# Kernel tuning notes

Hardware: AMD Instinct MI355X
Metric: run time of the kernel (lower is better)

The kernel has to match this reference:

```python
import jax, jax.numpy as jnp
import numpy as np

G = 64      # norm_groups
T = 5       # Newton-Schulz iterations
EPS = 1e-5


def setup_inputs() -> dict:
    key = jax.random.key(0)
    weight = jax.random.normal(key, (2048, 18432), dtype=jnp.float32)
    return {"weight": weight}


def reference(weight):
    out_ch = weight.shape[0]
    # Z: [G, c, d] with c = out_ch // G, d = prod(rest)
    Z = weight.reshape(G, out_ch // G, -1)
    Zc = Z - jnp.mean(Z, axis=-1, keepdims=True)
    # S = Zc @ Zc^T : [G, c, c]
    S = jnp.einsum('gcd,ged->gce', Zc, Zc)
    c = S.shape[-1]
    eye = jnp.eye(c, dtype=S.dtype)
    S = S + EPS * eye
    # Frobenius norm per group, keepdim -> [G,1,1]
    norm_S = jnp.sqrt(jnp.sum(S * S, axis=(1, 2), keepdims=True))
    S = S / norm_S
    # Newton-Schulz: B_{t+1} = 1.5*B_t - 0.5 * B_t^3 @ S
    B = jnp.broadcast_to(eye, S.shape)
    for _ in range(T):
        B3 = jnp.matmul(jnp.matmul(B, B), B)
        B = 1.5 * B - 0.5 * jnp.matmul(B3, S)
    W = jnp.matmul(B, Zc) / jnp.sqrt(norm_S)
    return W.reshape(weight.shape)
```

## Files before the change

kernel.cpp:

```cpp
#include <hip/hip_runtime.h>

#define G 64
#define C 32
#define D 18432
#define NCH 16
#define TD (D / NCH)
#define NST (TD / 128)
#define EPS 1e-5f
#define NS_ITERS 5

typedef __attribute__((ext_vector_type(8))) short short8v;
typedef __attribute__((ext_vector_type(4))) float float4v;

__device__ __forceinline__ void split3(float x, unsigned short& h1,
                                       unsigned short& h2, unsigned short& h3) {
    unsigned int u = __float_as_uint(x);
    unsigned int m1 = u & 0xffff0000u;
    float r1 = x - __uint_as_float(m1);
    unsigned int u2 = __float_as_uint(r1);
    unsigned int m2 = u2 & 0xffff0000u;
    float r2 = r1 - __uint_as_float(m2);
    h1 = (unsigned short)(m1 >> 16);
    h2 = (unsigned short)(m2 >> 16);
    h3 = (unsigned short)(__float_as_uint(r2) >> 16);
}

__device__ __forceinline__ void split8(const float4& v0, const float4& v1,
                                       short8v& p1, short8v& p2, short8v& p3,
                                       float& rs) {
    float x[8] = {v0.x, v0.y, v0.z, v0.w, v1.x, v1.y, v1.z, v1.w};
#pragma unroll
    for (int j = 0; j < 8; ++j) {
        unsigned short h1, h2, h3;
        rs += x[j];
        split3(x[j], h1, h2, h3);
        p1[j] = (short)h1; p2[j] = (short)h2; p3[j] = (short)h3;
    }
}

__global__ __launch_bounds__(256) void k1_gram(const float* __restrict__ W,
                                               float* __restrict__ psum,
                                               float* __restrict__ prow) {
    __shared__ float red[4 * 1056 + 4 * C];

    const int ch   = blockIdx.x;
    const int g    = blockIdx.y;
    const int bid  = g * NCH + ch;
    const int tid  = threadIdx.x;
    const int lane = tid & 63;
    const int wave = tid >> 6;

    const int rbase = lane & 15;
    const int koff  = (lane >> 4) * 8;

    const float* Zg = W + (size_t)g * C * D + (size_t)ch * TD;
    const float* p0 = Zg + (size_t)rbase * D + wave * 32 + koff;
    const float* p1 = p0 + (size_t)16 * D;

    float4v acc[2][2];
#pragma unroll
    for (int a = 0; a < 2; ++a)
#pragma unroll
        for (int b = 0; b < 2; ++b) acc[a][b] = (float4v)0.f;
    float rs0 = 0.f, rs1 = 0.f;

    float4 c00 = *(const float4*)(p0);
    float4 c01 = *(const float4*)(p0 + 4);
    float4 c10 = *(const float4*)(p1);
    float4 c11 = *(const float4*)(p1 + 4);

#pragma unroll
    for (int st = 0; st < NST; ++st) {
        float4 n00, n01, n10, n11;
        if (st + 1 < NST) {
            n00 = *(const float4*)(p0 + (st + 1) * 128);
            n01 = *(const float4*)(p0 + (st + 1) * 128 + 4);
            n10 = *(const float4*)(p1 + (st + 1) * 128);
            n11 = *(const float4*)(p1 + (st + 1) * 128 + 4);
        }
        short8v fa[3], fb[3];
        split8(c00, c01, fa[0], fa[1], fa[2], rs0);
        split8(c10, c11, fb[0], fb[1], fb[2], rs1);

        short8v* fr[2] = {fa, fb};
#pragma unroll
        for (int a = 0; a < 2; ++a)
#pragma unroll
            for (int b = 0; b < 2; ++b) {
                float4v t = acc[a][b];
                t = __builtin_amdgcn_mfma_f32_16x16x32_bf16(fr[a][0], fr[b][0], t, 0, 0, 0);
                t = __builtin_amdgcn_mfma_f32_16x16x32_bf16(fr[a][0], fr[b][1], t, 0, 0, 0);
                t = __builtin_amdgcn_mfma_f32_16x16x32_bf16(fr[a][1], fr[b][0], t, 0, 0, 0);
                t = __builtin_amdgcn_mfma_f32_16x16x32_bf16(fr[a][1], fr[b][1], t, 0, 0, 0);
                t = __builtin_amdgcn_mfma_f32_16x16x32_bf16(fr[a][0], fr[b][2], t, 0, 0, 0);
                t = __builtin_amdgcn_mfma_f32_16x16x32_bf16(fr[a][2], fr[b][0], t, 0, 0, 0);
                acc[a][b] = t;
            }
        c00 = n00; c01 = n01; c10 = n10; c11 = n11;
    }

    rs0 += __shfl_xor(rs0, 16, 64); rs0 += __shfl_xor(rs0, 32, 64);
    rs1 += __shfl_xor(rs1, 16, 64); rs1 += __shfl_xor(rs1, 32, 64);
    if (lane < 16) {
        red[4224 + wave * C + lane]      = rs0;
        red[4224 + wave * C + 16 + lane] = rs1;
    }

#pragma unroll
    for (int a = 0; a < 2; ++a)
#pragma unroll
        for (int b = 0; b < 2; ++b)
#pragma unroll
            for (int j = 0; j < 4; ++j) {
                int row = 16 * a + ((lane >> 4) << 2) + j;
                int col = 16 * b + (lane & 15);
                red[wave * 1056 + row * 33 + col] = acc[a][b][j];
            }
    __syncthreads();

#pragma unroll
    for (int k = 0; k < 4; ++k) {
        int el = tid + 256 * k;
        int row = el >> 5, col = el & 31;
        int o = row * 33 + col;
        float sv = red[o] + red[1056 + o] + red[2112 + o] + red[3168 + o];
        psum[(size_t)bid * (C * C) + el] = sv;
    }
    if (tid < C) {
        float s = red[4224 + tid] + red[4224 + C + tid] +
                  red[4224 + 2 * C + tid] + red[4224 + 3 * C + tid];
        prow[(size_t)bid * C + tid] = s;
    }
}

__global__ __launch_bounds__(256) void k2_ns(const float* __restrict__ psum,
                                             const float* __restrict__ prow,
                                             float* __restrict__ MT,
                                             float* __restrict__ vout) {
    __shared__ float S[C][C + 1];
    __shared__ float B[C][C + 1];
    __shared__ float T1[C][C + 1];
    __shared__ float T2[C][C + 1];
    __shared__ float mean[C];
    __shared__ float redw[4];
    __shared__ float normsh;

    const int g   = blockIdx.x;
    const int tid = threadIdx.x;
    const int e   = tid & 31;
    const int cbq = tid >> 5;

    float selt[4];
#pragma unroll
    for (int k = 0; k < 4; ++k) {
        int el = tid + 256 * k;
        float s = 0.f;
#pragma unroll
        for (int ch = 0; ch < NCH; ++ch)
            s += psum[((size_t)g * NCH + ch) * (C * C) + el];
        selt[k] = s;
    }
    if (tid < C) {
        float s = 0.f;
#pragma unroll
        for (int ch = 0; ch < NCH; ++ch)
            s += prow[((size_t)g * NCH + ch) * C + tid];
        mean[tid] = s / (float)D;
    }
    __syncthreads();

    float ss = 0.f;
#pragma unroll
    for (int k = 0; k < 4; ++k) {
        int el = tid + 256 * k;
        int c = el >> 5;
        float sv = selt[k] - (float)D * mean[c] * mean[e];
        if (c == e) sv += EPS;
        S[c][e] = sv;
        ss = fmaf(sv, sv, ss);
    }
#pragma unroll
    for (int off = 32; off >= 1; off >>= 1) ss += __shfl_xor(ss, off, 64);
    if ((tid & 63) == 0) redw[tid >> 6] = ss;
    __syncthreads();
    if (tid == 0) normsh = sqrtf(redw[0] + redw[1] + redw[2] + redw[3]);
    __syncthreads();
    const float inv_norm = 1.0f / normsh;
#pragma unroll
    for (int k = 0; k < 4; ++k) {
        int c = cbq + 8 * k;
        S[c][e] *= inv_norm;
        B[c][e] = (c == e) ? 1.f : 0.f;
    }
    __syncthreads();

    for (int it = 0; it < NS_ITERS; ++it) {
#pragma unroll
        for (int k = 0; k < 4; ++k) {
            int c = cbq + 8 * k;
            float s = 0.f;
            for (int kk = 0; kk < C; ++kk)
                s = fmaf(B[c][kk], B[kk][e], s);
            T1[c][e] = s;
        }
        __syncthreads();
#pragma unroll
        for (int k = 0; k < 4; ++k) {
            int c = cbq + 8 * k;
            float s = 0.f;
            for (int kk = 0; kk < C; ++kk)
                s = fmaf(T1[c][kk], B[kk][e], s);
            T2[c][e] = s;
        }
        __syncthreads();
        float pv[4];
#pragma unroll
        for (int k = 0; k < 4; ++k) {
            int c = cbq + 8 * k;
            float s = 0.f;
            for (int kk = 0; kk < C; ++kk)
                s = fmaf(T2[c][kk], S[kk][e], s);
            pv[k] = s;
        }
#pragma unroll
        for (int k = 0; k < 4; ++k) {
            int c = cbq + 8 * k;
            B[c][e] = 1.5f * B[c][e] - 0.5f * pv[k];
        }
        __syncthreads();
    }

    const float invs = 1.0f / sqrtf(normsh);
#pragma unroll
    for (int k = 0; k < 4; ++k) {
        int c = cbq + 8 * k;
        MT[(size_t)g * (C * C) + e * C + c] = B[c][e] * invs;
    }
    if (tid < C) {
        float s = 0.f;
        for (int ee = 0; ee < C; ++ee)
            s = fmaf(B[tid][ee] * invs, mean[ee], s);
        vout[(size_t)g * C + tid] = s;
    }
}

__global__ __launch_bounds__(256) void k3_apply(const float* __restrict__ W,
                                                const float* __restrict__ MT,
                                                const float* __restrict__ vv,
                                                float* __restrict__ out) {
    const int blocksPerGroup = D / 512;
    const int g   = blockIdx.x / blocksPerGroup;
    const int cbk = blockIdx.x % blocksPerGroup;
    const int d0  = cbk * 512 + (int)threadIdx.x * 2;
    const float* Zg = W + (size_t)g * C * D + d0;
    const float* Mg = MT + (size_t)g * (C * C);

    float accx[C], accy[C];
#pragma unroll
    for (int r = 0; r < C; ++r) { accx[r] = 0.f; accy[r] = 0.f; }

    for (int e = 0; e < C; ++e) {
        float2 z = *(const float2*)(Zg + (size_t)e * D);
#pragma unroll
        for (int r = 0; r < C; ++r) {
            float m = Mg[e * C + r];
            accx[r] = fmaf(m, z.x, accx[r]);
            accy[r] = fmaf(m, z.y, accy[r]);
        }
    }

    float* Og = out + (size_t)g * C * D + d0;
#pragma unroll
    for (int r = 0; r < C; ++r) {
        float vr = vv[g * C + r];
        float2 o = make_float2(accx[r] - vr, accy[r] - vr);
        double dv;
        __builtin_memcpy(&dv, &o, 8);
        __builtin_nontemporal_store(dv, (double*)(Og + (size_t)r * D));
    }
}

extern "C" void kernel_launch(void* const* d_in, const int* in_sizes, int n_in,
                              void* d_out, int out_size, void* d_ws, size_t ws_size,
                              hipStream_t stream) {
    const float* w = (const float*)d_in[0];
    float* out = (float*)d_out;

    float* psum = (float*)d_ws;
    float* prow = psum + (size_t)(G * NCH) * (C * C);
    float* MT   = prow + (size_t)(G * NCH) * C;
    float* vv   = MT   + (size_t)G * (C * C);

    k1_gram <<<dim3(NCH, G), 256, 0, stream>>>(w, psum, prow);
    k2_ns   <<<G,            256, 0, stream>>>(psum, prow, MT, vv);
    k3_apply<<<G * (D / 512), 256, 0, stream>>>(w, MT, vv, out);
}
```

Baseline: 92.04 us.

## Fuse Newton-Schulz stage into gram kernel via last-block atomic counter

Removes the separate Newton-Schulz kernel. The last block to finish each group's partial Gram sums, detected with a per-group atomic counter after a threadfence, reduces the partials and runs the iteration, reusing the reduction shared memory. A tiny zeroing kernel resets the counters each call. This saves one launch and lets the Newton-Schulz work for early groups overlap Gram computation for other groups. The cost is a serialized tail on the last block per group and reliance on fence ordering for correctness.

```diff
diff --git a/kernel.cpp b/kernel.cpp
--- a/kernel.cpp
+++ b/kernel.cpp
@@ -38,10 +38,19 @@
     }
 }
 
+__global__ void k0_zero(int* __restrict__ cnt) { cnt[threadIdx.x] = 0; }
+
 __global__ __launch_bounds__(256) void k1_gram(const float* __restrict__ W,
                                                float* __restrict__ psum,
-                                               float* __restrict__ prow) {
+                                               float* __restrict__ prow,
+                                               float* __restrict__ MT,
+                                               float* __restrict__ vout,
+                                               int* __restrict__ cnt) {
     __shared__ float red[4 * 1056 + 4 * C];
+    __shared__ float mean[C];
+    __shared__ float redw[4];
+    __shared__ float normsh;
+    __shared__ int lastFlag;
 
     const int ch   = blockIdx.x;
     const int g    = blockIdx.y;
@@ -131,116 +140,117 @@
                   red[4224 + 2 * C + tid] + red[4224 + 3 * C + tid];
         prow[(size_t)bid * C + tid] = s;
     }
-}
-
-__global__ __launch_bounds__(256) void k2_ns(const float* __restrict__ psum,
-                                             const float* __restrict__ prow,
-                                             float* __restrict__ MT,
-                                             float* __restrict__ vout) {
-    __shared__ float S[C][C + 1];
-    __shared__ float B[C][C + 1];
-    __shared__ float T1[C][C + 1];
-    __shared__ float T2[C][C + 1];
-    __shared__ float mean[C];
-    __shared__ float redw[4];
-    __shared__ float normsh;
-
-    const int g   = blockIdx.x;
-    const int tid = threadIdx.x;
-    const int e   = tid & 31;
-    const int cbq = tid >> 5;
-
-    float selt[4];
-#pragma unroll
-    for (int k = 0; k < 4; ++k) {
-        int el = tid + 256 * k;
-        float s = 0.f;
-#pragma unroll
-        for (int ch = 0; ch < NCH; ++ch)
-            s += psum[((size_t)g * NCH + ch) * (C * C) + el];
-        selt[k] = s;
-    }
-    if (tid < C) {
-        float s = 0.f;
-#pragma unroll
-        for (int ch = 0; ch < NCH; ++ch)
-            s += prow[((size_t)g * NCH + ch) * C + tid];
-        mean[tid] = s / (float)D;
-    }
+
     __syncthreads();
-
-    float ss = 0.f;
-#pragma unroll
-    for (int k = 0; k < 4; ++k) {
-        int el = tid + 256 * k;
-        int c = el >> 5;
-        float sv = selt[k] - (float)D * mean[c] * mean[e];
-        if (c == e) sv += EPS;
-        S[c][e] = sv;
-        ss = fmaf(sv, sv, ss);
-    }
-#pragma unroll
-    for (int off = 32; off >= 1; off >>= 1) ss += __shfl_xor(ss, off, 64);
-    if ((tid & 63) == 0) redw[tid >> 6] = ss;
+    if (tid == 0) {
+        __threadfence();
+        int old = atomicAdd(&cnt[g], 1);
+        lastFlag = (old == NCH - 1);
+    }
     __syncthreads();
-    if (tid == 0) normsh = sqrtf(redw[0] + redw[1] + redw[2] + redw[3]);
-    __syncthreads();
-    const float inv_norm = 1.0f / normsh;
-#pragma unroll
-    for (int k = 0; k < 4; ++k) {
-        int c = cbq + 8 * k;
-        S[c][e] *= inv_norm;
-        B[c][e] = (c == e) ? 1.f : 0.f;
-    }
-    __syncthreads();
-
-    for (int it = 0; it < NS_ITERS; ++it) {
+    if (!lastFlag) return;
+
+    __threadfence();
+    {
+        const int e   = tid & 31;
+        const int cbq = tid >> 5;
+        float* Sm  = red;
+        float* Bm  = red + 1056;
+        float* T1m = red + 2112;
+        float* T2m = red + 3168;
+
+        float selt[4];
+#pragma unroll
+        for (int k = 0; k < 4; ++k) {
+            int el = tid + 256 * k;
+            float s = 0.f;
+#pragma unroll
+            for (int c2 = 0; c2 < NCH; ++c2)
+                s += psum[((size_t)g * NCH + c2) * (C * C) + el];
+            selt[k] = s;
+        }
+        if (tid < C) {
+            float s = 0.f;
+#pragma unroll
+            for (int c2 = 0; c2 < NCH; ++c2)
+                s += prow[((size_t)g * NCH + c2) * C + tid];
+            mean[tid] = s / (float)D;
+        }
+        __syncthreads();
+
+        float ss = 0.f;
+#pragma unroll
+        for (int k = 0; k < 4; ++k) {
+            int el = tid + 256 * k;
+            int c = el >> 5;
+            float sv = selt[k] - (float)D * mean[c] * mean[e];
+            if (c == e) sv += EPS;
+            Sm[c * 33 + e] = sv;
+            ss = fmaf(sv, sv, ss);
+        }
+#pragma unroll
+        for (int off = 32; off >= 1; off >>= 1) ss += __shfl_xor(ss, off, 64);
+        if ((tid & 63) == 0) redw[tid >> 6] = ss;
+        __syncthreads();
+        if (tid == 0) normsh = sqrtf(redw[0] + redw[1] + redw[2] + redw[3]);
+        __syncthreads();
+        const float inv_norm = 1.0f / normsh;
 #pragma unroll
         for (int k = 0; k < 4; ++k) {
             int c = cbq + 8 * k;
-            float s = 0.f;
-            for (int kk = 0; kk < C; ++kk)
-                s = fmaf(B[c][kk], B[kk][e], s);
-            T1[c][e] = s;
+            Sm[c * 33 + e] *= inv_norm;
+            Bm[c * 33 + e] = (c == e) ? 1.f : 0.f;
         }
         __syncthreads();
+
+        for (int it = 0; it < NS_ITERS; ++it) {
+#pragma unroll
+            for (int k = 0; k < 4; ++k) {
+                int c = cbq + 8 * k;
+                float s = 0.f;
+                for (int kk = 0; kk < C; ++kk)
+                    s = fmaf(Bm[c * 33 + kk], Bm[kk * 33 + e], s);
+                T1m[c * 33 + e] = s;
+            }
+            __syncthreads();
+#pragma unroll
+            for (int k = 0; k < 4; ++k) {
+                int c = cbq + 8 * k;
+                float s = 0.f;
+                for (int kk = 0; kk < C; ++kk)
+                    s = fmaf(T1m[c * 33 + kk], Bm[kk * 33 + e], s);
+                T2m[c * 33 + e] = s;
+            }
+            __syncthreads();
+            float pv[4];
+#pragma unroll
+            for (int k = 0; k < 4; ++k) {
+                int c = cbq + 8 * k;
+                float s = 0.f;
+                for (int kk = 0; kk < C; ++kk)
+                    s = fmaf(T2m[c * 33 + kk], Sm[kk * 33 + e], s);
+                pv[k] = s;
+            }
+#pragma unroll
+            for (int k = 0; k < 4; ++k) {
+                int c = cbq + 8 * k;
+                Bm[c * 33 + e] = 1.5f * Bm[c * 33 + e] - 0.5f * pv[k];
+            }
+            __syncthreads();
+        }
+
+        const float invs = 1.0f / sqrtf(normsh);
 #pragma unroll
         for (int k = 0; k < 4; ++k) {
             int c = cbq + 8 * k;
+            MT[(size_t)g * (C * C) + e * C + c] = Bm[c * 33 + e] * invs;
+        }
+        if (tid < C) {
             float s = 0.f;
-            for (int kk = 0; kk < C; ++kk)
-                s = fmaf(T1[c][kk], B[kk][e], s);
-            T2[c][e] = s;
-        }
-        __syncthreads();
-        float pv[4];
-#pragma unroll
-        for (int k = 0; k < 4; ++k) {
-            int c = cbq + 8 * k;
-            float s = 0.f;
-            for (int kk = 0; kk < C; ++kk)
-                s = fmaf(T2[c][kk], S[kk][e], s);
-            pv[k] = s;
-        }
-#pragma unroll
-        for (int k = 0; k < 4; ++k) {
-            int c = cbq + 8 * k;
-            B[c][e] = 1.5f * B[c][e] - 0.5f * pv[k];
-        }
-        __syncthreads();
-    }
-
-    const float invs = 1.0f / sqrtf(normsh);
-#pragma unroll
-    for (int k = 0; k < 4; ++k) {
-        int c = cbq + 8 * k;
-        MT[(size_t)g * (C * C) + e * C + c] = B[c][e] * invs;
-    }
-    if (tid < C) {
-        float s = 0.f;
-        for (int ee = 0; ee < C; ++ee)
-            s = fmaf(B[tid][ee] * invs, mean[ee], s);
-        vout[(size_t)g * C + tid] = s;
+            for (int ee = 0; ee < C; ++ee)
+                s = fmaf(Bm[tid * 33 + ee] * invs, mean[ee], s);
+            vout[(size_t)g * C + tid] = s;
+        }
     }
 }
 
@@ -290,8 +300,9 @@
     float* prow = psum + (size_t)(G * NCH) * (C * C);
     float* MT   = prow + (size_t)(G * NCH) * C;
     float* vv   = MT   + (size_t)G * (C * C);
-
-    k1_gram <<<dim3(NCH, G), 256, 0, stream>>>(w, psum, prow);
-    k2_ns   <<<G,            256, 0, stream>>>(psum, prow, MT, vv);
+    int*   cnt  = (int*)(vv + (size_t)G * C);
+
+    k0_zero <<<1, G, 0, stream>>>(cnt);
+    k1_gram <<<dim3(NCH, G), 256, 0, stream>>>(w, psum, prow, MT, vv, cnt);
     k3_apply<<<G * (D / 512), 256, 0, stream>>>(w, MT, vv, out);
 }
```

After: 205.4 us. 123% more time.
